# Kernel optimization log

Hardware: AMD Instinct MI355X
Metric: run time of the kernel (lower is better)

The kernel has to match this reference:

```python
import jax, jax.numpy as jnp
import numpy as np

N_EMBD = 1024
N_HEAD = 16
HEAD_SIZE = N_EMBD // N_HEAD
EPS = 1e-5


def layer_norm(x, gamma, beta):
    mu = jnp.mean(x, axis=-1, keepdims=True)
    var = jnp.var(x, axis=-1, keepdims=True)
    return (x - mu) * jax.lax.rsqrt(var + EPS) * gamma + beta


def setup_inputs() -> dict:
    key = jax.random.key(0)
    ks = jax.random.split(key, 12)
    B, T, C, H, hs = 2, 2048, N_EMBD, N_HEAD, HEAD_SIZE
    s = lambda fan_in: 1.0 / np.sqrt(fan_in)
    return {
        "x": jax.random.normal(ks[0], (B, T, C), dtype=jnp.float32),
        "Wq": jax.random.normal(ks[1], (H, C, hs), dtype=jnp.float32) * s(C),
        "Wk": jax.random.normal(ks[2], (H, C, hs), dtype=jnp.float32) * s(C),
        "Wv": jax.random.normal(ks[3], (H, C, hs), dtype=jnp.float32) * s(C),
        "Wproj": jax.random.normal(ks[4], (C, C), dtype=jnp.float32) * s(C),
        "bproj": jax.random.normal(ks[5], (C,), dtype=jnp.float32) * 0.01,
        "g1": jnp.ones((C,), dtype=jnp.float32),
        "b1": jnp.zeros((C,), dtype=jnp.float32),
        "g2": jnp.ones((C,), dtype=jnp.float32),
        "b2": jnp.zeros((C,), dtype=jnp.float32),
        "W_ff1": jax.random.normal(ks[6], (C, 4 * C), dtype=jnp.float32) * s(C),
        "b_ff1": jax.random.normal(ks[7], (4 * C,), dtype=jnp.float32) * 0.01,
        "W_ff2": jax.random.normal(ks[8], (4 * C, C), dtype=jnp.float32) * s(4 * C),
        "b_ff2": jax.random.normal(ks[9], (C,), dtype=jnp.float32) * 0.01,
    }


def reference(x, Wq, Wk, Wv, Wproj, bproj, g1, b1, g2, b2, W_ff1, b_ff1, W_ff2, b_ff2):
    B, T, C = x.shape
    # --- LN1 + multi-head causal self-attention ---
    h = layer_norm(x, g1, b1)
    q = jnp.einsum("btc,hcd->bhtd", h, Wq)  # [B,H,T,hs]
    k = jnp.einsum("btc,hcd->bhtd", h, Wk)
    v = jnp.einsum("btc,hcd->bhtd", h, Wv)
    scale = HEAD_SIZE ** -0.5
    wei = jnp.einsum("bhtd,bhsd->bhts", q, k) * scale  # [B,H,T,T]
    mask = jnp.tril(jnp.ones((T, T), dtype=bool))
    wei = jnp.where(mask, wei, -jnp.inf)
    wei = jax.nn.softmax(wei, axis=-1)
    out = jnp.einsum("bhts,bhsd->bhtd", wei, v)  # [B,H,T,hs]
    out = out.transpose(0, 2, 1, 3).reshape(B, T, C)  # concat heads
    sa = out @ Wproj + bproj
    x = x + sa
    # --- LN2 + FFN ---
    h2 = layer_norm(x, g2, b2)
    ff = jax.nn.relu(h2 @ W_ff1 + b_ff1) @ W_ff2 + b_ff2
    return x + ff
```

## Files before the change

kernel.cpp:

```cpp
#include <hip/hip_runtime.h>
#include <hip/hip_bf16.h>

#define N_EMBD 1024
#define N_HEAD 16
#define HEADSZ 64
#define BATCH  2
#define SEQ    2048
#define ROWS   (BATCH*SEQ)

typedef __attribute__((ext_vector_type(8))) short bf16x8;
typedef __attribute__((ext_vector_type(4))) float f32x4;

__device__ __forceinline__ short f2bs(float v){
    union { __hip_bfloat16 b; short s; } u; u.b = __float2bfloat16(v); return u.s;
}
__device__ __forceinline__ short scale8th(short s){
    union { unsigned i; float f; } u; u.i = ((unsigned)(unsigned short)s) << 16;
    return f2bs(u.f * 0.125f);
}
__device__ __forceinline__ void gload16(const short* g, short* l){
    __builtin_amdgcn_global_load_lds(
        (const __attribute__((address_space(1))) unsigned int*)g,
        (__attribute__((address_space(3))) unsigned int*)l, 16, 0, 0);
}

__global__ __launch_bounds__(256) void tr_cvt(const float* __restrict__ in,
                                              short* __restrict__ out,
                                              int R, int Cc,
                                              size_t in_z, size_t out_z)
{
    __shared__ float t[32][33];
    const int tx = threadIdx.x & 31, ty = threadIdx.x >> 5;
    const int j0 = blockIdx.x * 32, i0 = blockIdx.y * 32;
    const float* ip = in + (size_t)blockIdx.z * in_z;
    short* op = out + (size_t)blockIdx.z * out_z;
#pragma unroll
    for (int p = 0; p < 4; ++p)
        t[ty + p * 8][tx] = ip[(size_t)(i0 + ty + p * 8) * Cc + j0 + tx];
    __syncthreads();
#pragma unroll
    for (int p = 0; p < 4; ++p)
        op[(size_t)(j0 + ty + p * 8) * R + i0 + tx] = f2bs(t[tx][ty + p * 8]);
}

__global__ __launch_bounds__(256) void tr3_cvt(const float* __restrict__ Wq,
                                               const float* __restrict__ Wk,
                                               const float* __restrict__ Wv,
                                               short* __restrict__ w2t)
{
    __shared__ float t[32][33];
    const int tx = threadIdx.x & 31, ty = threadIdx.x >> 5;
    const int which = blockIdx.z >> 4, head = blockIdx.z & 15;
    const int j0 = blockIdx.x * 32, i0 = blockIdx.y * 32;
    const float* ip = (which == 0 ? Wq : which == 1 ? Wk : Wv) + (size_t)head * 65536;
    short* op = w2t + (size_t)which * 1048576 + (size_t)head * 65536;
#pragma unroll
    for (int p = 0; p < 4; ++p)
        t[ty + p * 8][tx] = ip[(size_t)(i0 + ty + p * 8) * 64 + j0 + tx];
    __syncthreads();
#pragma unroll
    for (int p = 0; p < 4; ++p)
        op[(size_t)(j0 + ty + p * 8) * 1024 + i0 + tx] = f2bs(t[tx][ty + p * 8]);
}

__global__ __launch_bounds__(256) void vt_tr(const short* __restrict__ qkv,
                                             short* __restrict__ vt)
{
    __shared__ short t[64][65];
    const int tid = threadIdx.x;
    const int sr = tid >> 2, sc = (tid & 3) * 16;
    const int col0 = blockIdx.x * 64, tok0 = blockIdx.y * 64;
    const short* ip = qkv + (size_t)(tok0 + sr) * 3072 + 2048 + col0 + sc;
    bf16x8 v0 = *(const bf16x8*)ip;
    bf16x8 v1 = *(const bf16x8*)(ip + 8);
#pragma unroll
    for (int i = 0; i < 8; ++i) { t[sr][sc + i] = v0[i]; t[sr][sc + 8 + i] = v1[i]; }
    __syncthreads();
    bf16x8 a, bq;
#pragma unroll
    for (int i = 0; i < 8; ++i) { a[i] = t[sc + i][sr]; bq[i] = t[sc + 8 + i][sr]; }
    short* op = vt + (size_t)(col0 + sr) * 4096 + tok0 + sc;
    *(bf16x8*)op = a;
    *(bf16x8*)(op + 8) = bq;
}

__global__ __launch_bounds__(256) void ln_k(const float* __restrict__ x,
                                            const float* __restrict__ g,
                                            const float* __restrict__ bta,
                                            short* __restrict__ out)
{
    const int row = blockIdx.x;
    const int tid = threadIdx.x;
    const float* xr = x + (size_t)row * N_EMBD;
    float4 v = *(const float4*)(xr + tid * 4);
    float s  = v.x + v.y + v.z + v.w;
    float s2 = v.x * v.x + v.y * v.y + v.z * v.z + v.w * v.w;
#pragma unroll
    for (int off = 32; off; off >>= 1) {
        s  += __shfl_xor(s,  off, 64);
        s2 += __shfl_xor(s2, off, 64);
    }
    __shared__ float rs[4], rs2[4];
    const int wave = tid >> 6, lane = tid & 63;
    if (lane == 0) { rs[wave] = s; rs2[wave] = s2; }
    __syncthreads();
    s  = rs[0] + rs[1] + rs[2] + rs[3];
    s2 = rs2[0] + rs2[1] + rs2[2] + rs2[3];
    const float mean = s * (1.f / N_EMBD);
    const float var  = s2 * (1.f / N_EMBD) - mean * mean;
    const float rsig = rsqrtf(var + 1e-5f);
    float4 gv = *(const float4*)(g + tid * 4);
    float4 bv = *(const float4*)(bta + tid * 4);
    short4 o;
    o.x = f2bs((v.x - mean) * rsig * gv.x + bv.x);
    o.y = f2bs((v.y - mean) * rsig * gv.y + bv.y);
    o.z = f2bs((v.z - mean) * rsig * gv.z + bv.z);
    o.w = f2bs((v.w - mean) * rsig * gv.w + bv.w);
    *(short4*)(out + (size_t)row * N_EMBD + tid * 4) = o;
}

__global__ __launch_bounds__(256) void pln_fin(const float* __restrict__ p0,
                                               const float* __restrict__ p1,
                                               const float* __restrict__ bias,
                                               const float* __restrict__ x,
                                               const float* __restrict__ g,
                                               const float* __restrict__ bta,
                                               float* __restrict__ x2,
                                               short* __restrict__ h2)
{
    const int row = blockIdx.x, tid = threadIdx.x;
    const size_t base = (size_t)row * N_EMBD + tid * 4;
    float4 a  = *(const float4*)(p0 + base);
    float4 c  = *(const float4*)(p1 + base);
    float4 xx = *(const float4*)(x + base);
    float4 bb = *(const float4*)(bias + tid * 4);
    float4 v;
    v.x = a.x + c.x + xx.x + bb.x;
    v.y = a.y + c.y + xx.y + bb.y;
    v.z = a.z + c.z + xx.z + bb.z;
    v.w = a.w + c.w + xx.w + bb.w;
    *(float4*)(x2 + base) = v;
    float s  = v.x + v.y + v.z + v.w;
    float s2 = v.x * v.x + v.y * v.y + v.z * v.z + v.w * v.w;
#pragma unroll
    for (int off = 32; off; off >>= 1) {
        s  += __shfl_xor(s,  off, 64);
        s2 += __shfl_xor(s2, off, 64);
    }
    __shared__ float rs[4], rs2[4];
    const int wave = tid >> 6, lane = tid & 63;
    if (lane == 0) { rs[wave] = s; rs2[wave] = s2; }
    __syncthreads();
    s  = rs[0] + rs[1] + rs[2] + rs[3];
    s2 = rs2[0] + rs2[1] + rs2[2] + rs2[3];
    const float mean = s * (1.f / N_EMBD);
    const float var  = s2 * (1.f / N_EMBD) - mean * mean;
    const float rsig = rsqrtf(var + 1e-5f);
    float4 gv = *(const float4*)(g + tid * 4);
    float4 bv = *(const float4*)(bta + tid * 4);
    short4 o;
    o.x = f2bs((v.x - mean) * rsig * gv.x + bv.x);
    o.y = f2bs((v.y - mean) * rsig * gv.y + bv.y);
    o.z = f2bs((v.z - mean) * rsig * gv.z + bv.z);
    o.w = f2bs((v.w - mean) * rsig * gv.w + bv.w);
    *(short4*)(h2 + base) = o;
}

__global__ __launch_bounds__(256) void mfma_gemm(
    const short* __restrict__ A,
    const short* __restrict__ Bt,
    const float* __restrict__ bias,
    const float* __restrict__ resid,
    float* __restrict__ outf,
    float* __restrict__ outf2,
    short* __restrict__ outb,
    int M, int N, int K, int kz, int relu)
{
    __shared__ __align__(16) short As[3][128 * 32];
    __shared__ __align__(16) short Bs[3][128 * 32];
    const int tid  = threadIdx.x;
    const int lane = tid & 63, w = tid >> 6;
    const int quad = lane >> 4, l16 = lane & 15;
    const int row0 = blockIdx.y * 128, col0 = blockIdx.x * 128;
    const int wm = (w >> 1) * 64, wn = (w & 1) * 64;
    const int koff = blockIdx.z * kz;
    const int kend = kz ? kz : K;
    const int nk   = kend >> 5;

    f32x4 acc[4][4];
#pragma unroll
    for (int i = 0; i < 4; ++i)
#pragma unroll
        for (int j = 0; j < 4; ++j)
            acc[i][j] = f32x4{0.f, 0.f, 0.f, 0.f};

    const int c0  = w * 128 + lane;
    const int c1  = c0 + 64;
    const int ar0 = c0 >> 2, ak0 = (((c0 & 3) ^ ((ar0 >> 1) & 3))) * 8;
    const int ar1 = c1 >> 2, ak1 = (((c1 & 3) ^ ((ar1 >> 1) & 3))) * 8;
    const short* aG0 = A  + (size_t)(row0 + ar0) * K + koff + ak0;
    const short* aG1 = A  + (size_t)(row0 + ar1) * K + koff + ak1;
    const short* bG0 = Bt + (size_t)(col0 + ar0) * K + koff + ak0;
    const short* bG1 = Bt + (size_t)(col0 + ar1) * K + koff + ak1;
    const int lofs = w * 1024;

    const int gsw = (quad ^ ((l16 >> 1) & 3)) * 8;

    gload16(aG0, As[0] + lofs);
    gload16(aG1, As[0] + lofs + 512);
    gload16(bG0, Bs[0] + lofs);
    gload16(bG1, Bs[0] + lofs + 512);
    if (nk > 1) {
        gload16(aG0 + 32, As[1] + lofs);
        gload16(aG1 + 32, As[1] + lofs + 512);
        gload16(bG0 + 32, Bs[1] + lofs);
        gload16(bG1 + 32, Bs[1] + lofs + 512);
    }

    for (int k = 0; k < nk; ++k) {
        if (k + 1 < nk) asm volatile("s_waitcnt vmcnt(4)" ::: "memory");
        else            asm volatile("s_waitcnt vmcnt(0)" ::: "memory");
        __builtin_amdgcn_s_barrier();
        if (k + 2 < nk) {
            const int nb = (k + 2) % 3;
            const int ko = (k + 2) * 32;
            gload16(aG0 + ko, As[nb] + lofs);
            gload16(aG1 + ko, As[nb] + lofs + 512);
            gload16(bG0 + ko, Bs[nb] + lofs);
            gload16(bG1 + ko, Bs[nb] + lofs + 512);
        }
        const int cur = k % 3;

        bf16x8 af[4], bfr[4];
#pragma unroll
        for (int i = 0; i < 4; ++i)
            af[i]  = *(const bf16x8*)(As[cur] + (wm + i * 16 + l16) * 32 + gsw);
#pragma unroll
        for (int j = 0; j < 4; ++j)
            bfr[j] = *(const bf16x8*)(Bs[cur] + (wn + j * 16 + l16) * 32 + gsw);
#pragma unroll
        for (int i = 0; i < 4; ++i)
#pragma unroll
            for (int j = 0; j < 4; ++j)
                acc[i][j] = __builtin_amdgcn_mfma_f32_16x16x32_bf16(
                    af[i], bfr[j], acc[i][j], 0, 0, 0);
    }

    float* of = blockIdx.z ? outf2 : outf;
#pragma unroll
    for (int i = 0; i < 4; ++i) {
        const int rbase = row0 + wm + i * 16 + quad * 4;
#pragma unroll
        for (int j = 0; j < 4; ++j) {
            const int c = col0 + wn + j * 16 + l16;
            const float bv = bias ? bias[c] : 0.f;
#pragma unroll
            for (int r = 0; r < 4; ++r) {
                float v = acc[i][j][r] + bv;
                if (relu) v = fmaxf(v, 0.f);
                const size_t idx = (size_t)(rbase + r) * N + c;
                if (resid) v += resid[idx];
                if (outb) outb[idx] = f2bs(v);
                else      of[idx] = v;
            }
        }
    }
}

__global__ __launch_bounds__(512, 2) void mfma_gemm256(
    const short* __restrict__ A,
    const short* __restrict__ Bt,
    const float* __restrict__ bias,
    short* __restrict__ outb,
    int N, int K, int relu)
{
    __shared__ __align__(16) short As[2][256 * 32];
    __shared__ __align__(16) short Bs[2][256 * 32];
    const int tid  = threadIdx.x;
    const int lane = tid & 63, w = tid >> 6;
    const int quad = lane >> 4, l16 = lane & 15;
    const int row0 = blockIdx.y * 256, col0 = blockIdx.x * 256;
    const int wm = (w >> 2) * 128;
    const int wn = (w & 3) * 64;
    const int nk = K >> 5;

    f32x4 acc[8][4];
#pragma unroll
    for (int i = 0; i < 8; ++i)
#pragma unroll
        for (int j = 0; j < 4; ++j)
            acc[i][j] = f32x4{0.f, 0.f, 0.f, 0.f};

    const int i0 = tid, i1 = tid + 512;
    const int ar0 = i0 >> 2, ak0 = ((i0 & 3) ^ ((ar0 >> 1) & 3)) * 8;
    const int ar1 = i1 >> 2, ak1 = ((i1 & 3) ^ ((ar1 >> 1) & 3)) * 8;
    const short* aG0 = A  + (size_t)(row0 + ar0) * K + ak0;
    const short* aG1 = A  + (size_t)(row0 + ar1) * K + ak1;
    const short* bG0 = Bt + (size_t)(col0 + ar0) * K + ak0;
    const short* bG1 = Bt + (size_t)(col0 + ar1) * K + ak1;
    const int lofs = w * 512;

    const int gsw = (quad ^ ((l16 >> 1) & 3)) * 8;

    gload16(aG0, As[0] + lofs);
    gload16(aG1, As[0] + 4096 + lofs);
    gload16(bG0, Bs[0] + lofs);
    gload16(bG1, Bs[0] + 4096 + lofs);
    asm volatile("s_waitcnt vmcnt(0)" ::: "memory");
    __builtin_amdgcn_s_barrier();

    for (int k = 0; k < nk; ++k) {
        const int cur = k & 1;
        if (k + 1 < nk) {
            const int ko = (k + 1) * 32;
            const int nb = cur ^ 1;
            gload16(aG0 + ko, As[nb] + lofs);
            gload16(aG1 + ko, As[nb] + 4096 + lofs);
            gload16(bG0 + ko, Bs[nb] + lofs);
            gload16(bG1 + ko, Bs[nb] + 4096 + lofs);
        }

        bf16x8 af[8], bfr[4];
#pragma unroll
        for (int i = 0; i < 8; ++i)
            af[i]  = *(const bf16x8*)(As[cur] + (wm + i * 16 + l16) * 32 + gsw);
#pragma unroll
        for (int j = 0; j < 4; ++j)
            bfr[j] = *(const bf16x8*)(Bs[cur] + (wn + j * 16 + l16) * 32 + gsw);
#pragma unroll
        for (int i = 0; i < 8; ++i)
#pragma unroll
            for (int j = 0; j < 4; ++j)
                acc[i][j] = __builtin_amdgcn_mfma_f32_16x16x32_bf16(
                    af[i], bfr[j], acc[i][j], 0, 0, 0);

        asm volatile("s_waitcnt vmcnt(0)" ::: "memory");
        __builtin_amdgcn_s_barrier();
    }

#pragma unroll
    for (int i = 0; i < 8; ++i) {
        const int rbase = row0 + wm + i * 16 + quad * 4;
#pragma unroll
        for (int j = 0; j < 4; ++j) {
            const int c = col0 + wn + j * 16 + l16;
            const float bv = bias[c];
#pragma unroll
            for (int r = 0; r < 4; ++r) {
                float v = acc[i][j][r] + bv;
                if (relu) v = fmaxf(v, 0.f);
                outb[(size_t)(rbase + r) * N + c] = f2bs(v);
            }
        }
    }
}

__global__ __launch_bounds__(256) void mfma_gemm64(
    const short* __restrict__ A,
    const short* __restrict__ Bt,
    float* __restrict__ outf,
    float* __restrict__ outf2,
    int K, int kz)
{
    __shared__ __align__(16) short As[3][64 * 32];
    __shared__ __align__(16) short Bs[3][128 * 32];
    const int tid  = threadIdx.x;
    const int lane = tid & 63, w = tid >> 6;
    const int quad = lane >> 4, l16 = lane & 15;
    const int lin  = (int)blockIdx.y * 8 + (int)blockIdx.x;
    const int swz  = (lin & 7) * 64 + (lin >> 3);
    const int col0 = (swz & 7) * 128;
    const int row0 = (swz >> 3) * 64;
    const int wr = w >> 1, wc = w & 1;
    const int koff = blockIdx.z * kz;
    const int nk   = kz >> 5;

    f32x4 acc[2][4];
#pragma unroll
    for (int i = 0; i < 2; ++i)
#pragma unroll
        for (int j = 0; j < 4; ++j)
            acc[i][j] = f32x4{0.f, 0.f, 0.f, 0.f};

    const int ia  = w * 64 + lane;
    const int ar  = ia >> 2;
    const int aak = ((ia & 3) ^ ((ar >> 1) & 3)) * 8;
    const short* aG = A + (size_t)(row0 + ar) * K + koff + aak;
    const int aofs = w * 512;
    const int c0  = w * 128 + lane;
    const int c1  = c0 + 64;
    const int br0 = c0 >> 2, bk0 = ((c0 & 3) ^ ((br0 >> 1) & 3)) * 8;
    const int br1 = c1 >> 2, bk1 = ((c1 & 3) ^ ((br1 >> 1) & 3)) * 8;
    const short* bG0 = Bt + (size_t)(col0 + br0) * K + koff + bk0;
    const short* bG1 = Bt + (size_t)(col0 + br1) * K + koff + bk1;
    const int bofs = w * 1024;

    const int gsw = (quad ^ ((l16 >> 1) & 3)) * 8;

    gload16(aG, As[0] + aofs);
    gload16(bG0, Bs[0] + bofs);
    gload16(bG1, Bs[0] + bofs + 512);
    if (nk > 1) {
        gload16(aG + 32, As[1] + aofs);
        gload16(bG0 + 32, Bs[1] + bofs);
        gload16(bG1 + 32, Bs[1] + bofs + 512);
    }

    for (int k = 0; k < nk; ++k) {
        if (k + 1 < nk) asm volatile("s_waitcnt vmcnt(3)" ::: "memory");
        else            asm volatile("s_waitcnt vmcnt(0)" ::: "memory");
        __builtin_amdgcn_s_barrier();
        if (k + 2 < nk) {
            const int nb = (k + 2) % 3;
            const int ko = (k + 2) * 32;
            gload16(aG + ko, As[nb] + aofs);
            gload16(bG0 + ko, Bs[nb] + bofs);
            gload16(bG1 + ko, Bs[nb] + bofs + 512);
        }
        const int cur = k % 3;

        bf16x8 af[2], bfr[4];
#pragma unroll
        for (int i = 0; i < 2; ++i)
            af[i]  = *(const bf16x8*)(As[cur] + (wr * 32 + i * 16 + l16) * 32 + gsw);
#pragma unroll
        for (int j = 0; j < 4; ++j)
            bfr[j] = *(const bf16x8*)(Bs[cur] + (wc * 64 + j * 16 + l16) * 32 + gsw);
#pragma unroll
        for (int i = 0; i < 2; ++i)
#pragma unroll
            for (int j = 0; j < 4; ++j)
                acc[i][j] = __builtin_amdgcn_mfma_f32_16x16x32_bf16(
                    af[i], bfr[j], acc[i][j], 0, 0, 0);
    }

    float* of = blockIdx.z ? outf2 : outf;
#pragma unroll
    for (int i = 0; i < 2; ++i) {
        const int rbase = row0 + wr * 32 + i * 16 + quad * 4;
#pragma unroll
        for (int j = 0; j < 4; ++j) {
            const int c = col0 + wc * 64 + j * 16 + l16;
#pragma unroll
            for (int r = 0; r < 4; ++r)
                of[(size_t)(rbase + r) * 1024 + c] = acc[i][j][r];
        }
    }
}

__global__ __launch_bounds__(256) void ff2_fin(const float* __restrict__ p0,
                                               const float* __restrict__ bias,
                                               const float* __restrict__ x2,
                                               float* __restrict__ out)
{
    const size_t i = ((size_t)blockIdx.x * 256 + threadIdx.x) * 4;
    float4 a = *(const float4*)(p0 + i);
    float4 b = *(const float4*)(out + i);
    float4 r = *(const float4*)(x2 + i);
    float4 bb = *(const float4*)(bias + (i & 1023));
    float4 o;
    o.x = a.x + b.x + r.x + bb.x;
    o.y = a.y + b.y + r.y + bb.y;
    o.z = a.z + b.z + r.z + bb.z;
    o.w = a.w + b.w + r.w + bb.w;
    *(float4*)(out + i) = o;
}

__global__ __launch_bounds__(256) void attn_k(const short* __restrict__ qkv,
                                              const short* __restrict__ vt,
                                              short* __restrict__ att)
{
    __shared__ __align__(16) short Ks[2][64 * 64];
    __shared__ __align__(16) short Vs[2][64 * 64];
    __shared__ __align__(16) short Ps[64 * 64];
    const int tid  = threadIdx.x;
    const int lane = tid & 63, w = tid >> 6;
    const int quad = lane >> 4, l16 = lane & 15;
    const int bh = blockIdx.x, b = bh >> 4, head = bh & 15;

    const int srow = lane >> 3;
    const int sw   = ((lane & 7) ^ srow) * 8;
    const int cidx = (quad ^ (l16 & 7)) * 8;

#pragma unroll
    for (int pass = 0; pass < 2; ++pass) {
        const int qt = pass == 0 ? (int)blockIdx.y : 31 - (int)blockIdx.y;
        const int t0 = qt * 64;
        const int ntiles = qt + 1;

        const short* qp = qkv + (size_t)(b * SEQ + t0 + w * 16 + l16) * 3072
                          + head * 64 + quad * 8;
        bf16x8 qf0 = *(const bf16x8*)qp;
        bf16x8 qf1 = *(const bf16x8*)(qp + 32);
#pragma unroll
        for (int i = 0; i < 8; ++i) { qf0[i] = scale8th(qf0[i]); qf1[i] = scale8th(qf1[i]); }

        float mrow = -INFINITY, lrow = 0.f;
        f32x4 O[4];
#pragma unroll
        for (int jn = 0; jn < 4; ++jn) O[jn] = f32x4{0.f, 0.f, 0.f, 0.f};

        asm volatile("s_waitcnt vmcnt(0) lgkmcnt(0)\n\ts_barrier" ::: "memory");
        {
            const short* kg = qkv + (size_t)(b * SEQ + w * 16 + srow) * 3072
                              + 1024 + head * 64 + sw;
            const short* vg = vt + (size_t)(head * 64 + w * 16 + srow) * 4096
                              + b * SEQ + sw;
            short* kL = Ks[0] + w * 1024;
            short* vL = Vs[0] + w * 1024;
            gload16(kg, kL); gload16(kg + (size_t)8 * 3072, kL + 512);
            gload16(vg, vL); gload16(vg + (size_t)8 * 4096, vL + 512);
        }

        for (int kt = 0; kt < ntiles; ++kt) {
            const int cur = kt & 1;
            asm volatile("s_waitcnt vmcnt(0) lgkmcnt(0)\n\ts_barrier" ::: "memory");
            if (kt + 1 < ntiles) {
                const int s1 = (kt + 1) * 64;
                const short* kg = qkv + (size_t)(b * SEQ + s1 + w * 16 + srow) * 3072
                                  + 1024 + head * 64 + sw;
                const short* vg = vt + (size_t)(head * 64 + w * 16 + srow) * 4096
                                  + b * SEQ + s1 + sw;
                short* kL = Ks[cur ^ 1] + w * 1024;
                short* vL = Vs[cur ^ 1] + w * 1024;
                gload16(kg, kL); gload16(kg + (size_t)8 * 3072, kL + 512);
                gload16(vg, vL); gload16(vg + (size_t)8 * 4096, vL + 512);
            }

            f32x4 S[4];
            const short* Kb = Ks[cur];
#pragma unroll
            for (int jn = 0; jn < 4; ++jn) {
                S[jn] = f32x4{0.f, 0.f, 0.f, 0.f};
                const short* kp = Kb + (jn * 16 + l16) * 64;
                bf16x8 b0 = *(const bf16x8*)(kp + cidx);
                bf16x8 b1 = *(const bf16x8*)(kp + (cidx ^ 32));
                S[jn] = __builtin_amdgcn_mfma_f32_16x16x32_bf16(b0, qf0, S[jn], 0, 0, 0);
                S[jn] = __builtin_amdgcn_mfma_f32_16x16x32_bf16(b1, qf1, S[jn], 0, 0, 0);
            }

            float Sv[4][4];
            const int qrow = t0 + w * 16 + l16;
            const int s0 = kt * 64;
#pragma unroll
            for (int jn = 0; jn < 4; ++jn)
#pragma unroll
                for (int r = 0; r < 4; ++r)
                    Sv[jn][r] = S[jn][r];
            if (kt == ntiles - 1) {
#pragma unroll
                for (int jn = 0; jn < 4; ++jn)
#pragma unroll
                    for (int r = 0; r < 4; ++r)
                        if (s0 + jn * 16 + quad * 4 + r > qrow) Sv[jn][r] = -INFINITY;
            }
            float tmx[4];
#pragma unroll
            for (int jn = 0; jn < 4; ++jn)
                tmx[jn] = fmaxf(fmaxf(Sv[jn][0], Sv[jn][1]), fmaxf(Sv[jn][2], Sv[jn][3]));
            float pm = fmaxf(fmaxf(tmx[0], tmx[1]), fmaxf(tmx[2], tmx[3]));
            pm = fmaxf(pm, __shfl_xor(pm, 16, 64));
            pm = fmaxf(pm, __shfl_xor(pm, 32, 64));
            const float mn    = fmaxf(mrow, pm);
            const float alpha = __expf(mrow - mn);
#pragma unroll
            for (int jn = 0; jn < 4; ++jn)
#pragma unroll
                for (int r = 0; r < 4; ++r)
                    Sv[jn][r] = __expf(Sv[jn][r] - mn);
            float tsm[4];
#pragma unroll
            for (int jn = 0; jn < 4; ++jn)
                tsm[jn] = (Sv[jn][0] + Sv[jn][1]) + (Sv[jn][2] + Sv[jn][3]);
            float ps = (tsm[0] + tsm[1]) + (tsm[2] + tsm[3]);
            ps += __shfl_xor(ps, 16, 64);
            ps += __shfl_xor(ps, 32, 64);
            lrow = lrow * alpha + ps;
            mrow = mn;
#pragma unroll
            for (int r = 0; r < 4; ++r) {
                const float a = __shfl(alpha, quad * 4 + r, 64);
#pragma unroll
                for (int jn = 0; jn < 4; ++jn) O[jn][r] *= a;
            }

#pragma unroll
            for (int jn = 0; jn < 4; ++jn) {
                short4 pv;
                pv.x = f2bs(Sv[jn][0]); pv.y = f2bs(Sv[jn][1]);
                pv.z = f2bs(Sv[jn][2]); pv.w = f2bs(Sv[jn][3]);
                const int prow = w * 16 + l16;
                const int pcol = jn * 16 + quad * 4;
                const int chunk = (pcol >> 3) ^ (l16 & 7);
                *(short4*)(Ps + prow * 64 + chunk * 8 + (pcol & 7)) = pv;
            }
            asm volatile("s_waitcnt lgkmcnt(0)" ::: "memory");

            const short* pp = Ps + (w * 16 + l16) * 64;
            bf16x8 pf0 = *(const bf16x8*)(pp + cidx);
            bf16x8 pf1 = *(const bf16x8*)(pp + (cidx ^ 32));
            const short* Vb = Vs[cur];
#pragma unroll
            for (int jn = 0; jn < 4; ++jn) {
                const short* vp = Vb + (jn * 16 + l16) * 64;
                bf16x8 v0 = *(const bf16x8*)(vp + cidx);
                bf16x8 v1 = *(const bf16x8*)(vp + (cidx ^ 32));
                O[jn] = __builtin_amdgcn_mfma_f32_16x16x32_bf16(pf0, v0, O[jn], 0, 0, 0);
                O[jn] = __builtin_amdgcn_mfma_f32_16x16x32_bf16(pf1, v1, O[jn], 0, 0, 0);
            }
        }

#pragma unroll
        for (int r = 0; r < 4; ++r) {
            const float lr  = __shfl(lrow, quad * 4 + r, 64);
            const float inv = 1.f / lr;
            const size_t rowoff = (size_t)(b * SEQ + t0 + w * 16 + quad * 4 + r) * N_EMBD
                                  + head * 64 + l16;
#pragma unroll
            for (int jn = 0; jn < 4; ++jn)
                att[rowoff + jn * 16] = f2bs(O[jn][r] * inv);
        }
    }
}

extern "C" void kernel_launch(void* const* d_in, const int* in_sizes, int n_in,
                              void* d_out, int out_size, void* d_ws, size_t ws_size,
                              hipStream_t stream)
{
    const float* x     = (const float*)d_in[0];
    const float* Wq    = (const float*)d_in[1];
    const float* Wk    = (const float*)d_in[2];
    const float* Wv    = (const float*)d_in[3];
    const float* Wproj = (const float*)d_in[4];
    const float* bproj = (const float*)d_in[5];
    const float* g1    = (const float*)d_in[6];
    const float* b1    = (const float*)d_in[7];
    const float* g2    = (const float*)d_in[8];
    const float* b2    = (const float*)d_in[9];
    const float* Wff1  = (const float*)d_in[10];
    const float* bff1  = (const float*)d_in[11];
    const float* Wff2  = (const float*)d_in[12];
    const float* bff2  = (const float*)d_in[13];
    float* out = (float*)d_out;

    char* ws = (char*)d_ws;
    short* w2t  = (short*)(ws + 0);
    short* wpt  = (short*)(ws + 6291456);
    short* wf1t = (short*)(ws + 8388608);
    short* wf2t = (short*)(ws + 16777216);
    short* h    = (short*)(ws + 25165824);
    short* qkv  = (short*)(ws + 33554432);
    short* vt   = (short*)(ws + 58720256);
    short* att  = (short*)(ws + 67108864);
    float* x2   = (float*)(ws + 75497472);
    short* h2   = h;
    float* p0p  = (float*)(ws + 33554432);
    float* p1p  = (float*)(ws + 50331648);
    short* ff   = qkv;
    float* p0f  = (float*)(ws + 0);

    tr3_cvt<<<dim3(2, 32, 48),  256, 0, stream>>>(Wq, Wk, Wv, w2t);
    tr_cvt<<<dim3(32, 32, 1),  256, 0, stream>>>(Wproj, wpt,  1024, 1024, 0, 0);
    tr_cvt<<<dim3(128, 32, 1), 256, 0, stream>>>(Wff1, wf1t,  1024, 4096, 0, 0);
    tr_cvt<<<dim3(32, 128, 1), 256, 0, stream>>>(Wff2, wf2t,  4096, 1024, 0, 0);

    ln_k<<<ROWS, 256, 0, stream>>>(x, g1, b1, h);
    mfma_gemm<<<dim3(3072 / 128, ROWS / 128), 256, 0, stream>>>(
        h, w2t, nullptr, nullptr, nullptr, nullptr, qkv, ROWS, 3072, N_EMBD, 0, 0);
    vt_tr<<<dim3(16, 64), 256, 0, stream>>>(qkv, vt);
    attn_k<<<dim3(BATCH * N_HEAD, 16), 256, 0, stream>>>(qkv, vt, att);
    mfma_gemm64<<<dim3(8, 64, 2), 256, 0, stream>>>(att, wpt, p0p, p1p, N_EMBD, 512);
    pln_fin<<<ROWS, 256, 0, stream>>>(p0p, p1p, bproj, x, g2, b2, x2, h2);
    mfma_gemm256<<<dim3(4096 / 256, ROWS / 256), 512, 0, stream>>>(
        h2, wf1t, bff1, ff, 4096, N_EMBD, 1);
    mfma_gemm64<<<dim3(8, 64, 2), 256, 0, stream>>>(ff, wf2t, p0f, out, 4096, 2048);
    ff2_fin<<<ROWS * N_EMBD / 1024, 256, 0, stream>>>(p0f, bff2, x2, out);
}
```

Baseline: 362.0 us.

## Fuse V transpose into QKV GEMM epilogue and skip rare softmax rescales

The QKV GEMM epilogue now writes the V columns straight into the transposed vt buffer, which removes the separate vt_tr kernel launch and its global round trip. The attention kernel also adopts lazy rescaling: when the new tile max exceeds the running max by no more than 8 anywhere in the wave, it keeps the old max and skips the alpha exp and the O rescale. This saves ALU work and shuffles per tile but allows exp values up to e^8 in bf16 P and the fp32 accumulators. The transposed stores from the epilogue are short4 writes with a 4096 stride, so they are poorly coalesced.

Measured after the change: 358.6 us. Within noise of the previous version (-0.9%).

```diff
diff --git a/kernel.cpp b/kernel.cpp
--- a/kernel.cpp
+++ b/kernel.cpp
@@ -61,27 +61,6 @@
 #pragma unroll
     for (int p = 0; p < 4; ++p)
         op[(size_t)(j0 + ty + p * 8) * 1024 + i0 + tx] = f2bs(t[tx][ty + p * 8]);
-}
-
-__global__ __launch_bounds__(256) void vt_tr(const short* __restrict__ qkv,
-                                             short* __restrict__ vt)
-{
-    __shared__ short t[64][65];
-    const int tid = threadIdx.x;
-    const int sr = tid >> 2, sc = (tid & 3) * 16;
-    const int col0 = blockIdx.x * 64, tok0 = blockIdx.y * 64;
-    const short* ip = qkv + (size_t)(tok0 + sr) * 3072 + 2048 + col0 + sc;
-    bf16x8 v0 = *(const bf16x8*)ip;
-    bf16x8 v1 = *(const bf16x8*)(ip + 8);
-#pragma unroll
-    for (int i = 0; i < 8; ++i) { t[sr][sc + i] = v0[i]; t[sr][sc + 8 + i] = v1[i]; }
-    __syncthreads();
-    bf16x8 a, bq;
-#pragma unroll
-    for (int i = 0; i < 8; ++i) { a[i] = t[sc + i][sr]; bq[i] = t[sc + 8 + i][sr]; }
-    short* op = vt + (size_t)(col0 + sr) * 4096 + tok0 + sc;
-    *(bf16x8*)op = a;
-    *(bf16x8*)(op + 8) = bq;
 }
 
 __global__ __launch_bounds__(256) void ln_k(const float* __restrict__ x,
@@ -174,6 +153,7 @@
     float* __restrict__ outf,
     float* __restrict__ outf2,
     short* __restrict__ outb,
+    short* __restrict__ vtout,
     int M, int N, int K, int kz, int relu)
 {
     __shared__ __align__(16) short As[3][128 * 32];
@@ -244,6 +224,22 @@
             for (int j = 0; j < 4; ++j)
                 acc[i][j] = __builtin_amdgcn_mfma_f32_16x16x32_bf16(
                     af[i], bfr[j], acc[i][j], 0, 0, 0);
+    }
+
+    if (vtout && col0 >= 2048) {
+#pragma unroll
+        for (int i = 0; i < 4; ++i) {
+            const int rbase = row0 + wm + i * 16 + quad * 4;
+#pragma unroll
+            for (int j = 0; j < 4; ++j) {
+                const int c = col0 + wn + j * 16 + l16 - 2048;
+                short4 pv;
+                pv.x = f2bs(acc[i][j][0]); pv.y = f2bs(acc[i][j][1]);
+                pv.z = f2bs(acc[i][j][2]); pv.w = f2bs(acc[i][j][3]);
+                *(short4*)(vtout + (size_t)c * 4096 + rbase) = pv;
+            }
+        }
+        return;
     }
 
     float* of = blockIdx.z ? outf2 : outf;
@@ -561,8 +557,9 @@
             float pm = fmaxf(fmaxf(tmx[0], tmx[1]), fmaxf(tmx[2], tmx[3]));
             pm = fmaxf(pm, __shfl_xor(pm, 16, 64));
             pm = fmaxf(pm, __shfl_xor(pm, 32, 64));
-            const float mn    = fmaxf(mrow, pm);
-            const float alpha = __expf(mrow - mn);
+
+            const bool skip = __all(pm - mrow <= 8.f);
+            const float mn = skip ? mrow : fmaxf(mrow, pm);
 #pragma unroll
             for (int jn = 0; jn < 4; ++jn)
 #pragma unroll
@@ -575,13 +572,18 @@
             float ps = (tsm[0] + tsm[1]) + (tsm[2] + tsm[3]);
             ps += __shfl_xor(ps, 16, 64);
             ps += __shfl_xor(ps, 32, 64);
-            lrow = lrow * alpha + ps;
-            mrow = mn;
-#pragma unroll
-            for (int r = 0; r < 4; ++r) {
-                const float a = __shfl(alpha, quad * 4 + r, 64);
-#pragma unroll
-                for (int jn = 0; jn < 4; ++jn) O[jn][r] *= a;
+            if (skip) {
+                lrow += ps;
+            } else {
+                const float alpha = __expf(mrow - mn);
+                lrow = lrow * alpha + ps;
+                mrow = mn;
+#pragma unroll
+                for (int r = 0; r < 4; ++r) {
+                    const float a = __shfl(alpha, quad * 4 + r, 64);
+#pragma unroll
+                    for (int jn = 0; jn < 4; ++jn) O[jn][r] *= a;
+                }
             }
 
 #pragma unroll
@@ -666,8 +668,8 @@
 
     ln_k<<<ROWS, 256, 0, stream>>>(x, g1, b1, h);
     mfma_gemm<<<dim3(3072 / 128, ROWS / 128), 256, 0, stream>>>(
-        h, w2t, nullptr, nullptr, nullptr, nullptr, qkv, ROWS, 3072, N_EMBD, 0, 0);
-    vt_tr<<<dim3(16, 64), 256, 0, stream>>>(qkv, vt);
+        h, w2t, nullptr, nullptr, nullptr, nullptr, qkv, vt,
+        ROWS, 3072, N_EMBD, 0, 0);
     attn_k<<<dim3(BATCH * N_HEAD, 16), 256, 0, stream>>>(qkv, vt, att);
     mfma_gemm64<<<dim3(8, 64, 2), 256, 0, stream>>>(att, wpt, p0p, p1p, N_EMBD, 512);
     pln_fin<<<ROWS, 256, 0, stream>>>(p0p, p1p, bproj, x, g2, b2, x2, h2);
```
